# Optimization experiments

Measured on AMD Instinct MI355X. Metric: run time of the kernel, lower is better.

Reference implementation:

```python
import jax, jax.numpy as jnp
import numpy as np
from jax import lax

B, L = 8192, 64
N_VALUES, EMBED, HIDDEN, OUT = 1000, 64, 128, 128


def setup_inputs() -> dict:
    key = jax.random.key(0)
    ks = jax.random.split(key, 8)
    s = 0.1  # weight scale ~ 1/sqrt(hidden)
    return {
        "x": jax.random.randint(ks[0], (B, L), 0, N_VALUES),
        "embed": jax.random.normal(ks[1], (N_VALUES, EMBED), jnp.float32) * s,
        "W_ih": jax.random.normal(ks[2], (3 * HIDDEN, EMBED), jnp.float32) * s,
        "W_hh": jax.random.normal(ks[3], (3 * HIDDEN, HIDDEN), jnp.float32) * s,
        "b_ih": jax.random.normal(ks[4], (3 * HIDDEN,), jnp.float32) * s,
        "b_hh": jax.random.normal(ks[5], (3 * HIDDEN,), jnp.float32) * s,
        "W_out": jax.random.normal(ks[6], (OUT, HIDDEN), jnp.float32) * s,
        "b_out": jax.random.normal(ks[7], (OUT,), jnp.float32) * s,
    }


def _gru_encode(x, embed, W_ih, W_hh, b_ih, b_hh, W_out, b_out):
    e = embed[x]  # [B, L, E] embedding lookup
    H = W_hh.shape[1]
    # Precompute input-to-gate projections for all timesteps (batched GEMM).
    xg = jnp.einsum('ble,ge->blg', e, W_ih) + b_ih  # [B, L, 3H]

    def step(h, xg_t):
        hg = h @ W_hh.T + b_hh  # [B, 3H]
        xr, xz, xn = jnp.split(xg_t, 3, axis=-1)
        hr, hz, hn = jnp.split(hg, 3, axis=-1)
        r = jax.nn.sigmoid(xr + hr)
        z = jax.nn.sigmoid(xz + hz)
        n = jnp.tanh(xn + r * hn)  # PyTorch GRU: r gates the hidden 'new' term
        h_new = (1.0 - z) * n + z * h
        return h_new, None

    h0 = jnp.zeros((x.shape[0], H), e.dtype)
    h_last, _ = lax.scan(step, h0, jnp.swapaxes(xg, 0, 1))  # scan over time
    return h_last @ W_out.T + b_out  # [B, OUT]


def reference(x, embed, W_ih, W_hh, b_ih, b_hh, W_out, b_out):
    return _gru_encode(x, embed, W_ih, W_hh, b_ih, b_hh, W_out, b_out)
```

## Files before the change

kernel.cpp:

```cpp
#include <hip/hip_runtime.h>


typedef __bf16 bf16x8 __attribute__((ext_vector_type(8)));
typedef float  f32x4  __attribute__((ext_vector_type(4)));

#define NV   1000
#define EMB  64
#define HD   128
#define G3   384
#define SEQ  64
#define BB   32

__device__ __forceinline__ float sigm_f(float x) {
    return __builtin_amdgcn_rcpf(1.f + __builtin_amdgcn_exp2f(-1.44269504088896f * x));
}
__device__ __forceinline__ float tanh_f(float x) {
    return 1.f - 2.f * __builtin_amdgcn_rcpf(1.f + __builtin_amdgcn_exp2f(2.88539008177793f * x));
}

__global__ void g_table_kernel(const float* __restrict__ embed,
                               const float* __restrict__ W_ih,
                               const float* __restrict__ b_ih,
                               const float* __restrict__ b_hh,
                               float* __restrict__ Gt)
{
    __shared__ float emb[EMB];
    const int v = blockIdx.x;
    const int g = threadIdx.x;
    if (g < EMB) emb[g] = embed[v * EMB + g];
    __syncthreads();
    const float* wr = W_ih + g * EMB;
    float s = b_ih[g] + (g < 2 * HD ? b_hh[g] : 0.f);
    #pragma unroll
    for (int e = 0; e < EMB; e += 4) {
        const float4 w4 = *(const float4*)(wr + e);
        s += w4.x * emb[e] + w4.y * emb[e + 1] + w4.z * emb[e + 2] + w4.w * emb[e + 3];
    }
    Gt[v * G3 + g] = s;
}

__global__ __launch_bounds__(512, 2) void gru_kernel(
    const int*   __restrict__ x,    const float* __restrict__ Gt,
    const float* __restrict__ Whh,  const float* __restrict__ bhh,
    const float* __restrict__ Wout, const float* __restrict__ bout,
    float* __restrict__ out)
{
    __shared__ unsigned short hA[BB * HD];
    __shared__ int xl[BB * SEQ];

    const int tid  = threadIdx.x;
    const int lane = tid & 63;
    const int wid  = tid >> 6;
    const int cw   = wid & 3;
    const int rw   = wid >> 2;
    const int c16  = lane & 15;
    const int quad = lane >> 4;
    const int br0  = blockIdx.x * BB;

    #pragma unroll
    for (int i = 0; i < (BB * SEQ) / 512; ++i)
        xl[tid + i * 512] = x[br0 * SEQ + tid + i * 512];

    #pragma unroll
    for (int i = 0; i < (BB * HD) / (512 * 2); ++i)
        ((unsigned int*)hA)[tid + i * 512] = 0u;

    bf16x8 wf[3][2][4];
    #pragma unroll
    for (int gate = 0; gate < 3; ++gate)
    #pragma unroll
    for (int ht = 0; ht < 2; ++ht)
    #pragma unroll
    for (int ks = 0; ks < 4; ++ks) {
        const int col = gate * HD + cw * 32 + ht * 16 + c16;
        const float* p = Whh + col * HD + ks * 32 + quad * 4;
        const float4 a = *(const float4*)p;
        const float4 b = *(const float4*)(p + 16);
        bf16x8 f;
        f[0] = (__bf16)a.x; f[1] = (__bf16)a.y; f[2] = (__bf16)a.z; f[3] = (__bf16)a.w;
        f[4] = (__bf16)b.x; f[5] = (__bf16)b.y; f[6] = (__bf16)b.z; f[7] = (__bf16)b.w;
        wf[gate][ht][ks] = f;
    }
    bf16x8 wo[2][4];
    #pragma unroll
    for (int ht = 0; ht < 2; ++ht)
    #pragma unroll
    for (int ks = 0; ks < 4; ++ks) {
        const int col = cw * 32 + ht * 16 + c16;
        const float* p = Wout + col * HD + ks * 32 + quad * 4;
        const float4 a = *(const float4*)p;
        const float4 b = *(const float4*)(p + 16);
        bf16x8 f;
        f[0] = (__bf16)a.x; f[1] = (__bf16)a.y; f[2] = (__bf16)a.z; f[3] = (__bf16)a.w;
        f[4] = (__bf16)b.x; f[5] = (__bf16)b.y; f[6] = (__bf16)b.z; f[7] = (__bf16)b.w;
        wo[ht][ks] = f;
    }

    const float bn0 = bhh[2 * HD + cw * 32 + c16];
    const float bn1 = bhh[2 * HD + cw * 32 + 16 + c16];
    const float bo0 = bout[cw * 32 + c16];
    const float bo1 = bout[cw * 32 + 16 + c16];

    float hreg[2][4] = {{0.f,0.f,0.f,0.f},{0.f,0.f,0.f,0.f}};

    __syncthreads();

    float pf[3][2][4];
    {
        int tok[4];
        #pragma unroll
        for (int j = 0; j < 4; ++j)
            tok[j] = xl[(rw * 16 + quad * 4 + j) * SEQ + 0];
        #pragma unroll
        for (int j = 0; j < 4; ++j) {
            const float* gp = Gt + tok[j] * G3 + cw * 32 + c16;
            #pragma unroll
            for (int gate = 0; gate < 3; ++gate) {
                pf[gate][0][j] = gp[gate * HD];
                pf[gate][1][j] = gp[gate * HD + 16];
            }
        }
    }

    const f32x4 z4 = {0.f, 0.f, 0.f, 0.f};

    for (int t = 0; t < SEQ; ++t) {
        f32x4 acc[3][2];
        #pragma unroll
        for (int g2 = 0; g2 < 3; ++g2) { acc[g2][0] = z4; acc[g2][1] = z4; }
        #pragma unroll
        for (int ks = 0; ks < 4; ++ks) {
            const int arow = rw * 16 + c16;
            const int aoff = arow * 256 + ((ks * 64 + quad * 16) ^ ((arow & 7) << 4));
            const bf16x8 af = *(const bf16x8*)((const char*)hA + aoff);
            #pragma unroll
            for (int gate = 0; gate < 3; ++gate)
            #pragma unroll
            for (int ht = 0; ht < 2; ++ht)
                acc[gate][ht] = __builtin_amdgcn_mfma_f32_16x16x32_bf16(
                    af, wf[gate][ht][ks], acc[gate][ht], 0, 0, 0);
        }

        unsigned short hbits[2][4];
        #pragma unroll
        for (int ht = 0; ht < 2; ++ht) {
            const float bn_ = ht ? bn1 : bn0;
            #pragma unroll
            for (int j = 0; j < 4; ++j) {
                const float r  = sigm_f(pf[0][ht][j] + acc[0][ht][j]);
                const float zg = sigm_f(pf[1][ht][j] + acc[1][ht][j]);
                const float n  = tanh_f(pf[2][ht][j] + r * (acc[2][ht][j] + bn_));
                const float hp = hreg[ht][j];
                const float hn = zg * (hp - n) + n;
                hreg[ht][j] = hn;
                hbits[ht][j] = __builtin_bit_cast(unsigned short, (__bf16)hn);
            }
        }

        if (t + 1 < SEQ) {
            int tok[4];
            #pragma unroll
            for (int j = 0; j < 4; ++j)
                tok[j] = xl[(rw * 16 + quad * 4 + j) * SEQ + t + 1];
            #pragma unroll
            for (int j = 0; j < 4; ++j) {
                const float* gp = Gt + tok[j] * G3 + cw * 32 + c16;
                #pragma unroll
                for (int gate = 0; gate < 3; ++gate) {
                    pf[gate][0][j] = gp[gate * HD];
                    pf[gate][1][j] = gp[gate * HD + 16];
                }
            }
        }

        __syncthreads();

        #pragma unroll
        for (int ht = 0; ht < 2; ++ht) {
            const int hid  = cw * 32 + ht * 16 + c16;
            const int sidx = ((hid >> 5) << 5) + (((hid & 15) >> 2) << 3)
                           + (((hid >> 4) & 1) << 2) + (hid & 3);
            #pragma unroll
            for (int j = 0; j < 4; ++j) {
                const int row = rw * 16 + quad * 4 + j;
                const int off = row * 256 + ((sidx * 2) ^ ((row & 7) << 4));
                *(unsigned short*)((char*)hA + off) = hbits[ht][j];
            }
        }
        __syncthreads();
    }

    f32x4 oacc[2] = {z4, z4};
    #pragma unroll
    for (int ks = 0; ks < 4; ++ks) {
        const int arow = rw * 16 + c16;
        const int aoff = arow * 256 + ((ks * 64 + quad * 16) ^ ((arow & 7) << 4));
        const bf16x8 af = *(const bf16x8*)((const char*)hA + aoff);
        #pragma unroll
        for (int ht = 0; ht < 2; ++ht)
            oacc[ht] = __builtin_amdgcn_mfma_f32_16x16x32_bf16(af, wo[ht][ks], oacc[ht], 0, 0, 0);
    }
    #pragma unroll
    for (int ht = 0; ht < 2; ++ht) {
        const float bo_ = ht ? bo1 : bo0;
        #pragma unroll
        for (int j = 0; j < 4; ++j) {
            const int row = br0 + rw * 16 + quad * 4 + j;
            out[row * HD + cw * 32 + ht * 16 + c16] = oacc[ht][j] + bo_;
        }
    }
}

extern "C" void kernel_launch(void* const* d_in, const int* in_sizes, int n_in,
                              void* d_out, int out_size, void* d_ws, size_t ws_size,
                              hipStream_t stream) {
    const int*   x     = (const int*)  d_in[0];
    const float* embed = (const float*)d_in[1];
    const float* W_ih  = (const float*)d_in[2];
    const float* W_hh  = (const float*)d_in[3];
    const float* b_ih  = (const float*)d_in[4];
    const float* b_hh  = (const float*)d_in[5];
    const float* W_out = (const float*)d_in[6];
    const float* b_out = (const float*)d_in[7];
    float* outp = (float*)d_out;
    float* Gt   = (float*)d_ws;

    const int Bsz = in_sizes[0] / SEQ;

    g_table_kernel<<<NV, G3, 0, stream>>>(embed, W_ih, b_ih, b_hh, Gt);
    gru_kernel<<<Bsz / BB, 512, 0, stream>>>(x, Gt, W_hh, b_hh, W_out, b_out, outp);
}
```

Baseline: 108.3 us.

## Double-buffer hidden state, pack gate table in bf16, shrink batch tile to 16

The hidden state in LDS is now double-buffered, so each timestep needs a single barrier instead of two. The precomputed input-gate table is stored as bf16 in a per-lane packed layout, so one 16-byte load fetches all six gate values a lane needs. Blocks now cover 16 rows with 256 threads, which doubles the grid to 512 blocks and gives better CU coverage. The costs are bf16 rounding of the input projections and more blocks each reloading the W_hh fragments.

Result: slower. 118.3 us (+9.3%).

```diff
diff --git a/kernel.cpp b/kernel.cpp
--- a/kernel.cpp
+++ b/kernel.cpp
@@ -3,26 +3,33 @@
 
 typedef __bf16 bf16x8 __attribute__((ext_vector_type(8)));
 typedef float  f32x4  __attribute__((ext_vector_type(4)));
+typedef int    int4v  __attribute__((ext_vector_type(4)));
+typedef unsigned int uint4v __attribute__((ext_vector_type(4)));
 
 #define NV   1000
 #define EMB  64
 #define HD   128
 #define G3   384
 #define SEQ  64
-#define BB   32
+#define BB   16
 
 __device__ __forceinline__ float sigm_f(float x) {
     return __builtin_amdgcn_rcpf(1.f + __builtin_amdgcn_exp2f(-1.44269504088896f * x));
 }
 __device__ __forceinline__ float tanh_f(float x) {
     return 1.f - 2.f * __builtin_amdgcn_rcpf(1.f + __builtin_amdgcn_exp2f(2.88539008177793f * x));
+}
+__device__ __forceinline__ float bfslot(uint4v w, int s) {
+    const unsigned int word = w[s >> 1];
+    const unsigned int bits = (s & 1) ? (word & 0xffff0000u) : (word << 16);
+    return __builtin_bit_cast(float, bits);
 }
 
 __global__ void g_table_kernel(const float* __restrict__ embed,
                                const float* __restrict__ W_ih,
                                const float* __restrict__ b_ih,
                                const float* __restrict__ b_hh,
-                               float* __restrict__ Gt)
+                               unsigned short* __restrict__ Gpk)
 {
     __shared__ float emb[EMB];
     const int v = blockIdx.x;
@@ -36,34 +43,76 @@
         const float4 w4 = *(const float4*)(wr + e);
         s += w4.x * emb[e] + w4.y * emb[e + 1] + w4.z * emb[e + 2] + w4.w * emb[e + 3];
     }
-    Gt[v * G3 + g] = s;
-}
-
-__global__ __launch_bounds__(512, 2) void gru_kernel(
-    const int*   __restrict__ x,    const float* __restrict__ Gt,
+    const int hid = g & 127, gate = g >> 7;
+    const int cwi = hid >> 5, hti = (hid >> 4) & 1, c16i = hid & 15;
+    Gpk[((v * 4 + cwi) * 16 + c16i) * 8 + (gate + 3 * hti)] =
+        __builtin_bit_cast(unsigned short, (__bf16)s);
+}
+
+#define GRU_STEP(P, PFU, PFN, T)                                                   \
+  {                                                                                \
+    int4v tokn = {0, 0, 0, 0};                                                     \
+    if ((T) < SEQ - 1) tokn = *(const int4v*)&xl[((T) + 1) * BB + quad * 4];       \
+    f32x4 acc[3][2];                                                               \
+    _Pragma("unroll") for (int g2 = 0; g2 < 3; ++g2) {                             \
+      acc[g2][0] = z4; acc[g2][1] = z4;                                            \
+    }                                                                              \
+    _Pragma("unroll") for (int ks = 0; ks < 4; ++ks) {                             \
+      const bf16x8 af = *(const bf16x8*)(hbase + (P) * 4096 + aoff[ks]);           \
+      _Pragma("unroll") for (int gate = 0; gate < 3; ++gate)                       \
+        _Pragma("unroll") for (int ht = 0; ht < 2; ++ht)                           \
+          acc[gate][ht] = __builtin_amdgcn_mfma_f32_16x16x32_bf16(                 \
+              af, wf[gate][ht][ks], acc[gate][ht], 0, 0, 0);                       \
+    }                                                                              \
+    if ((T) < SEQ - 1) {                                                           \
+      _Pragma("unroll") for (int j = 0; j < 4; ++j)                                \
+        PFN[j] = *(const uint4v*)(gbase + (unsigned)(tokn[j] * 1024 + goff));      \
+    }                                                                              \
+    _Pragma("unroll") for (int ht = 0; ht < 2; ++ht) {                             \
+      const float bn_ = ht ? bn1 : bn0;                                            \
+      _Pragma("unroll") for (int j = 0; j < 4; ++j) {                              \
+        const float xr = bfslot(PFU[j], 3 * ht + 0);                               \
+        const float xz = bfslot(PFU[j], 3 * ht + 1);                               \
+        const float xn = bfslot(PFU[j], 3 * ht + 2);                               \
+        const float r  = sigm_f(xr + acc[0][ht][j]);                               \
+        const float zg = sigm_f(xz + acc[1][ht][j]);                               \
+        const float n  = tanh_f(xn + r * (acc[2][ht][j] + bn_));                   \
+        const float hn = zg * (hreg[ht][j] - n) + n;                               \
+        hreg[ht][j] = hn;                                                          \
+        *(unsigned short*)(hbase + (1 - (P)) * 4096 + woff[ht][j]) =               \
+            __builtin_bit_cast(unsigned short, (__bf16)hn);                        \
+      }                                                                            \
+    }                                                                              \
+    asm volatile("s_waitcnt lgkmcnt(0)" ::: "memory");                             \
+    __builtin_amdgcn_s_barrier();                                                  \
+    __builtin_amdgcn_sched_barrier(0);                                             \
+  }
+
+__global__ __launch_bounds__(256, 2) void gru_kernel(
+    const int*   __restrict__ x,    const unsigned short* __restrict__ Gpk,
     const float* __restrict__ Whh,  const float* __restrict__ bhh,
     const float* __restrict__ Wout, const float* __restrict__ bout,
     float* __restrict__ out)
 {
-    __shared__ unsigned short hA[BB * HD];
-    __shared__ int xl[BB * SEQ];
+    __shared__ unsigned short hA[2 * BB * HD];
+    __shared__ int xl[SEQ * BB];
 
     const int tid  = threadIdx.x;
     const int lane = tid & 63;
-    const int wid  = tid >> 6;
-    const int cw   = wid & 3;
-    const int rw   = wid >> 2;
+    const int cw   = tid >> 6;
     const int c16  = lane & 15;
     const int quad = lane >> 4;
     const int br0  = blockIdx.x * BB;
 
     #pragma unroll
-    for (int i = 0; i < (BB * SEQ) / 512; ++i)
-        xl[tid + i * 512] = x[br0 * SEQ + tid + i * 512];
-
-    #pragma unroll
-    for (int i = 0; i < (BB * HD) / (512 * 2); ++i)
-        ((unsigned int*)hA)[tid + i * 512] = 0u;
+    for (int i = 0; i < 4; ++i) {
+        const int r = (tid >> 6) + i * 4;
+        const int t = tid & 63;
+        xl[t * BB + r] = x[(br0 + r) * SEQ + t];
+    }
+    #pragma unroll
+    for (int i = 0; i < 4; ++i)
+        ((unsigned int*)hA)[tid + i * 256] = 0u;
 
     bf16x8 wf[3][2][4];
     #pragma unroll
@@ -81,6 +130,48 @@
         f[4] = (__bf16)b.x; f[5] = (__bf16)b.y; f[6] = (__bf16)b.z; f[7] = (__bf16)b.w;
         wf[gate][ht][ks] = f;
     }
+
+    const float bn0 = bhh[2 * HD + cw * 32 + c16];
+    const float bn1 = bhh[2 * HD + cw * 32 + 16 + c16];
+
+    int aoff[4];
+    #pragma unroll
+    for (int ks = 0; ks < 4; ++ks)
+        aoff[ks] = c16 * 256 + ((ks * 64 + quad * 16) ^ ((c16 & 7) << 4));
+    int woff[2][4];
+    #pragma unroll
+    for (int ht = 0; ht < 2; ++ht)
+    #pragma unroll
+    for (int j = 0; j < 4; ++j) {
+        const int hid  = cw * 32 + ht * 16 + c16;
+        const int sidx = ((hid >> 5) << 5) | (((hid & 15) >> 2) << 3)
+                       | (((hid >> 4) & 1) << 2) | (hid & 3);
+        const int row  = quad * 4 + j;
+        woff[ht][j] = row * 256 + ((sidx * 2) ^ ((row & 7) << 4));
+    }
+
+    char* hbase = (char*)hA;
+    const char* gbase = (const char*)Gpk;
+    const int goff = cw * 256 + c16 * 16;
+
+    float hreg[2][4] = {{0.f, 0.f, 0.f, 0.f}, {0.f, 0.f, 0.f, 0.f}};
+    const f32x4 z4 = {0.f, 0.f, 0.f, 0.f};
+
+    __syncthreads();
+
+    uint4v pfA[4], pfB[4];
+    {
+        const int4v tok0 = *(const int4v*)&xl[0 * BB + quad * 4];
+        #pragma unroll
+        for (int j = 0; j < 4; ++j)
+            pfA[j] = *(const uint4v*)(gbase + (unsigned)(tok0[j] * 1024 + goff));
+    }
+
+    for (int tt = 0; tt < SEQ; tt += 2) {
+        GRU_STEP(0, pfA, pfB, tt);
+        GRU_STEP(1, pfB, pfA, tt + 1);
+    }
+
     bf16x8 wo[2][4];
     #pragma unroll
     for (int ht = 0; ht < 2; ++ht)
@@ -95,107 +186,13 @@
         f[4] = (__bf16)b.x; f[5] = (__bf16)b.y; f[6] = (__bf16)b.z; f[7] = (__bf16)b.w;
         wo[ht][ks] = f;
     }
-
-    const float bn0 = bhh[2 * HD + cw * 32 + c16];
-    const float bn1 = bhh[2 * HD + cw * 32 + 16 + c16];
     const float bo0 = bout[cw * 32 + c16];
     const float bo1 = bout[cw * 32 + 16 + c16];
 
-    float hreg[2][4] = {{0.f,0.f,0.f,0.f},{0.f,0.f,0.f,0.f}};
-
-    __syncthreads();
-
-    float pf[3][2][4];
-    {
-        int tok[4];
-        #pragma unroll
-        for (int j = 0; j < 4; ++j)
-            tok[j] = xl[(rw * 16 + quad * 4 + j) * SEQ + 0];
-        #pragma unroll
-        for (int j = 0; j < 4; ++j) {
-            const float* gp = Gt + tok[j] * G3 + cw * 32 + c16;
-            #pragma unroll
-            for (int gate = 0; gate < 3; ++gate) {
-                pf[gate][0][j] = gp[gate * HD];
-                pf[gate][1][j] = gp[gate * HD + 16];
-            }
-        }
-    }
-
-    const f32x4 z4 = {0.f, 0.f, 0.f, 0.f};
-
-    for (int t = 0; t < SEQ; ++t) {
-        f32x4 acc[3][2];
-        #pragma unroll
-        for (int g2 = 0; g2 < 3; ++g2) { acc[g2][0] = z4; acc[g2][1] = z4; }
-        #pragma unroll
-        for (int ks = 0; ks < 4; ++ks) {
-            const int arow = rw * 16 + c16;
-            const int aoff = arow * 256 + ((ks * 64 + quad * 16) ^ ((arow & 7) << 4));
-            const bf16x8 af = *(const bf16x8*)((const char*)hA + aoff);
-            #pragma unroll
-            for (int gate = 0; gate < 3; ++gate)
-            #pragma unroll
-            for (int ht = 0; ht < 2; ++ht)
-                acc[gate][ht] = __builtin_amdgcn_mfma_f32_16x16x32_bf16(
-                    af, wf[gate][ht][ks], acc[gate][ht], 0, 0, 0);
-        }
-
-        unsigned short hbits[2][4];
-        #pragma unroll
-        for (int ht = 0; ht < 2; ++ht) {
-            const float bn_ = ht ? bn1 : bn0;
-            #pragma unroll
-            for (int j = 0; j < 4; ++j) {
-                const float r  = sigm_f(pf[0][ht][j] + acc[0][ht][j]);
-                const float zg = sigm_f(pf[1][ht][j] + acc[1][ht][j]);
-                const float n  = tanh_f(pf[2][ht][j] + r * (acc[2][ht][j] + bn_));
-                const float hp = hreg[ht][j];
-                const float hn = zg * (hp - n) + n;
-                hreg[ht][j] = hn;
-                hbits[ht][j] = __builtin_bit_cast(unsigned short, (__bf16)hn);
-            }
-        }
-
-        if (t + 1 < SEQ) {
-            int tok[4];
-            #pragma unroll
-            for (int j = 0; j < 4; ++j)
-                tok[j] = xl[(rw * 16 + quad * 4 + j) * SEQ + t + 1];
-            #pragma unroll
-            for (int j = 0; j < 4; ++j) {
-                const float* gp = Gt + tok[j] * G3 + cw * 32 + c16;
-                #pragma unroll
-                for (int gate = 0; gate < 3; ++gate) {
-                    pf[gate][0][j] = gp[gate * HD];
-                    pf[gate][1][j] = gp[gate * HD + 16];
-                }
-            }
-        }
-
-        __syncthreads();
-
-        #pragma unroll
-        for (int ht = 0; ht < 2; ++ht) {
-            const int hid  = cw * 32 + ht * 16 + c16;
-            const int sidx = ((hid >> 5) << 5) + (((hid & 15) >> 2) << 3)
-                           + (((hid >> 4) & 1) << 2) + (hid & 3);
-            #pragma unroll
-            for (int j = 0; j < 4; ++j) {
-                const int row = rw * 16 + quad * 4 + j;
-                const int off = row * 256 + ((sidx * 2) ^ ((row & 7) << 4));
-                *(unsigned short*)((char*)hA + off) = hbits[ht][j];
-            }
-        }
-        __syncthreads();
-    }
-
     f32x4 oacc[2] = {z4, z4};
     #pragma unroll
     for (int ks = 0; ks < 4; ++ks) {
-        const int arow = rw * 16 + c16;
-        const int aoff = arow * 256 + ((ks * 64 + quad * 16) ^ ((arow & 7) << 4));
-        const bf16x8 af = *(const bf16x8*)((const char*)hA + aoff);
+        const bf16x8 af = *(const bf16x8*)(hbase + aoff[ks]);
         #pragma unroll
         for (int ht = 0; ht < 2; ++ht)
             oacc[ht] = __builtin_amdgcn_mfma_f32_16x16x32_bf16(af, wo[ht][ks], oacc[ht], 0, 0, 0);
@@ -205,7 +202,7 @@
         const float bo_ = ht ? bo1 : bo0;
         #pragma unroll
         for (int j = 0; j < 4; ++j) {
-            const int row = br0 + rw * 16 + quad * 4 + j;
+            const int row = br0 + quad * 4 + j;
             out[row * HD + cw * 32 + ht * 16 + c16] = oacc[ht][j] + bo_;
         }
     }
@@ -223,10 +220,10 @@
     const float* W_out = (const float*)d_in[6];
     const float* b_out = (const float*)d_in[7];
     float* outp = (float*)d_out;
-    float* Gt   = (float*)d_ws;
+    unsigned short* Gpk = (unsigned short*)d_ws;
 
     const int Bsz = in_sizes[0] / SEQ;
 
-    g_table_kernel<<<NV, G3, 0, stream>>>(embed, W_ih, b_ih, b_hh, Gt);
-    gru_kernel<<<Bsz / BB, 512, 0, stream>>>(x, Gt, W_hh, b_hh, W_out, b_out, outp);
-}
+    g_table_kernel<<<NV, G3, 0, stream>>>(embed, W_ih, b_ih, b_hh, Gpk);
+    gru_kernel<<<Bsz / BB, 256, 0, stream>>>(x, Gpk, W_hh, b_hh, W_out, b_out, outp);
+}
```
